# Performance work log

Hardware: AMD Instinct MI355X
Metric: run time of the kernel (lower is better)

The kernel has to match this reference:

```python
import jax, jax.numpy as jnp
import numpy as np


def setup_inputs() -> dict:
    key = jax.random.key(0)
    k1, k2 = jax.random.split(key)
    B, T, F = 8, 1000, 257
    m = jax.random.normal(k1, (B, 27, T, F), dtype=jnp.float32)
    x = jax.random.normal(k2, (B, F, T, 2), dtype=jnp.float32)
    v = jnp.array([[1.0, -0.5, -0.5], [0.0, np.sqrt(3) / 2, -np.sqrt(3) / 2]], dtype=jnp.float32)
    return {"m": m, "x": x, "v": v}


def reference(m, x, v):
    B, C, T, F = m.shape
    # m -> (B, 3, 9, T, F); contract the complex-basis dim (3) with v rows
    m5 = m.reshape(B, 3, C // 3, T, F)
    H_real = jnp.einsum('k,bkntf->bntf', v[0], m5)  # (B, 9, T, F)
    H_imag = jnp.einsum('k,bkntf->bntf', v[1], m5)
    M_real = H_real.reshape(B, 3, 3, T, F)
    M_imag = H_imag.reshape(B, 3, 3, T, F)

    # x: (B,F,T,2) -> (B,2,T,F), pad: time causal (top=2), freq symmetric (1,1)
    xp = jnp.transpose(x, (0, 3, 2, 1))
    xp = jnp.pad(xp, ((0, 0), (0, 0), (2, 0), (1, 1)))
    # 3x3 unfold as 9 shifted views: (B, 2, 3, 3, T, F)
    xu = jnp.stack(
        [xp[:, :, i:i + T, j:j + F] for i in range(3) for j in range(3)],
        axis=2,
    ).reshape(B, 2, 3, 3, T, F)

    xr, xi = xu[:, 0], xu[:, 1]
    x_enh_real = jnp.sum(M_real * xr - M_imag * xi, axis=(1, 2))  # (B, T, F)
    x_enh_imag = jnp.sum(M_real * xi + M_imag * xr, axis=(1, 2))
    x_enh = jnp.stack([x_enh_real, x_enh_imag], axis=3)  # (B, T, F, 2)
    return jnp.transpose(x_enh, (0, 2, 1, 3))  # (B, F, T, 2)
```

## Files before the change

### kernel.cpp

```cpp
#include <hip/hip_runtime.h>


constexpr int B = 8, C = 27, T = 1000, F = 257;
constexpr int TCH = 8;
constexpr int NT  = T / TCH;
constexpr int GRP = 320;
constexpr int BLK = 3 * GRP;
constexpr int HROW = 6;
constexpr int RP   = 7;
constexpr int PLANE = 260 * RP;
constexpr int SLABP = 257;
constexpr size_t CS = (size_t)T * F;

__global__ __launch_bounds__(BLK, 8)
void ccm_kernel(const float* __restrict__ m,
                const float* __restrict__ x,
                float* __restrict__ out) {
    __shared__ float  xs[2 * PLANE];
    __shared__ float2 rs[3 * TCH * SLABP];

    const int bid = blockIdx.x;
    const int tc  = bid % NT;
    const int b   = bid / NT;
    const int t0  = tc * TCH;
    const int tx  = threadIdx.x;
    const int g   = tx / GRP;
    const int f   = tx - g * GRP;
    const bool active = (f < F);

    const float* xb = x + (size_t)b * F * T * 2;

    const float SQ3_2 = 0.8660254037844386f;
    const float ckr = (g == 0) ? 1.0f : -0.5f;
    const float cki = (g == 0) ? 0.0f : ((g == 1) ? SQ3_2 : -SQ3_2);

    const float* mb = m + (((size_t)b * C + 9 * g) * T + t0) * F;

    float Am[9], Bm[9];
    float wr[3][3], wi[3][3];

    auto stage = [&](int tb) {
        for (int p = tx; p < 259 * HROW; p += BLK) {
            const int row = p / HROW;
            const int tt  = p - row * HROW;
            const int ff  = row - 1;
            const int t   = tb + tt;
            float re = 0.f, im = 0.f;
            if (ff >= 0 && ff < F && t >= 0) {
                const float2 v = *reinterpret_cast<const float2*>(
                    xb + ((size_t)ff * T + t) * 2);
                re = v.x; im = v.y;
            }
            xs[row * RP + tt]         = re;
            xs[PLANE + row * RP + tt] = im;
        }
    };

#define LOADM(DST, S)                                                     \
    {                                                                     \
        _Pragma("unroll")                                                 \
        for (int n = 0; n < 9; ++n)                                       \
            DST[n] = mb[(size_t)n * CS + (size_t)(S) * F + f];            \
    }

#define STEP(AV, S, U)                                                    \
    {                                                                     \
        _Pragma("unroll")                                                 \
        for (int j = 0; j < 3; ++j) {                                     \
            const float xr = xs[(f + j) * RP + ((U) + 2)];                \
            const float xi = xs[PLANE + (f + j) * RP + ((U) + 2)];        \
            wr[2][j] = ckr * xr - cki * xi;                               \
            wi[2][j] = ckr * xi + cki * xr;                               \
        }                                                                 \
        float accr = 0.f, acci = 0.f;                                     \
        _Pragma("unroll")                                                 \
        for (int i = 0; i < 3; ++i) {                                     \
            _Pragma("unroll")                                             \
            for (int j = 0; j < 3; ++j) {                                 \
                const int n = i * 3 + j;                                  \
                accr += AV[n] * wr[i][j];                                 \
                acci += AV[n] * wi[i][j];                                 \
            }                                                             \
        }                                                                 \
        rs[g * (TCH * SLABP) + (S) * SLABP + f] = make_float2(accr, acci);\
        _Pragma("unroll")                                                 \
        for (int j = 0; j < 3; ++j) {                                     \
            wr[0][j] = wr[1][j]; wi[0][j] = wi[1][j];                     \
            wr[1][j] = wr[2][j]; wi[1][j] = wi[2][j];                     \
        }                                                                 \
    }

    if (active) {
        LOADM(Am, 0);
        LOADM(Bm, 1);
    }
    stage(t0 - 2);
    __syncthreads();

    if (active) {
        #pragma unroll
        for (int p = 0; p < 2; ++p) {
            #pragma unroll
            for (int j = 0; j < 3; ++j) {
                const float xr = xs[(f + j) * RP + p];
                const float xi = xs[PLANE + (f + j) * RP + p];
                wr[p][j] = ckr * xr - cki * xi;
                wi[p][j] = ckr * xi + cki * xr;
            }
        }
        STEP(Am, 0, 0);  LOADM(Am, 2);
        STEP(Bm, 1, 1);  LOADM(Bm, 3);
        STEP(Am, 2, 2);  LOADM(Am, 4);
        STEP(Bm, 3, 3);  LOADM(Bm, 5);
    }
    __syncthreads();

    stage(t0 + 2);
    __syncthreads();

    if (active) {
        STEP(Am, 4, 0);  LOADM(Am, 6);
        STEP(Bm, 5, 1);  LOADM(Bm, 7);
        STEP(Am, 6, 2);
        STEP(Bm, 7, 3);
    }
#undef LOADM
#undef STEP
    __syncthreads();

    for (int task = tx; task < F * 4; task += BLK) {
        const int ff = task >> 2;
        const int q  = task & 3;
        float4 o = make_float4(0.f, 0.f, 0.f, 0.f);
        #pragma unroll
        for (int gg = 0; gg < 3; ++gg) {
            const float2 p0 = rs[gg * (TCH * SLABP) + (2 * q) * SLABP + ff];
            const float2 p1 = rs[gg * (TCH * SLABP) + (2 * q + 1) * SLABP + ff];
            o.x += p0.x; o.y += p0.y; o.z += p1.x; o.w += p1.y;
        }
        *reinterpret_cast<float4*>(
            out + ((size_t)(b * F + ff) * T + t0) * 2 + q * 4) = o;
    }
}

extern "C" void kernel_launch(void* const* d_in, const int* in_sizes, int n_in,
                              void* d_out, int out_size, void* d_ws, size_t ws_size,
                              hipStream_t stream) {
    const float* m = (const float*)d_in[0];
    const float* x = (const float*)d_in[1];
    float* out = (float*)d_out;

    const int grid = B * NT;
    ccm_kernel<<<grid, BLK, 0, stream>>>(m, x, out);
}
```

Baseline: 66.14 us.

## Halve time chunk per block and stage the x halo in a single pass

The time chunk per block drops from 8 to 4 steps, which doubles the grid and removes the second x-staging phase along with its extra barriers. The x halo (6 time rows) is loaded once at kernel start and overlaps with the m register prefetches. A third register buffer lets three m slices be in flight at once. In exchange, x halo reuse per block falls and there are twice as many blocks to launch.

```diff
diff --git a/kernel.cpp b/kernel.cpp
--- a/kernel.cpp
+++ b/kernel.cpp
@@ -2,12 +2,13 @@
 
 
 constexpr int B = 8, C = 27, T = 1000, F = 257;
-constexpr int TCH = 8;
+constexpr int TCH = 4;
 constexpr int NT  = T / TCH;
 constexpr int GRP = 320;
 constexpr int BLK = 3 * GRP;
-constexpr int HROW = 6;
-constexpr int RP   = 7;
+constexpr int TROW  = TCH + 2;
+constexpr int ROWSU = 259;
+constexpr int RP    = 7;
 constexpr int PLANE = 260 * RP;
 constexpr int SLABP = 257;
 constexpr size_t CS = (size_t)T * F;
@@ -30,31 +31,29 @@
 
     const float* xb = x + (size_t)b * F * T * 2;
 
+    for (int p = tx; p < ROWSU * TROW; p += BLK) {
+        const int row = p / TROW;
+        const int tt  = p - row * TROW;
+        const int ff  = row - 1;
+        const int t   = t0 - 2 + tt;
+        float re = 0.f, im = 0.f;
+        if (ff >= 0 && ff < F && t >= 0) {
+            const float2 v = *reinterpret_cast<const float2*>(
+                xb + ((size_t)ff * T + t) * 2);
+            re = v.x; im = v.y;
+        }
+        xs[row * RP + tt]         = re;
+        xs[PLANE + row * RP + tt] = im;
+    }
+
     const float SQ3_2 = 0.8660254037844386f;
     const float ckr = (g == 0) ? 1.0f : -0.5f;
     const float cki = (g == 0) ? 0.0f : ((g == 1) ? SQ3_2 : -SQ3_2);
 
     const float* mb = m + (((size_t)b * C + 9 * g) * T + t0) * F;
 
-    float Am[9], Bm[9];
+    float Am[9], Bm[9], Cm[9];
     float wr[3][3], wi[3][3];
-
-    auto stage = [&](int tb) {
-        for (int p = tx; p < 259 * HROW; p += BLK) {
-            const int row = p / HROW;
-            const int tt  = p - row * HROW;
-            const int ff  = row - 1;
-            const int t   = tb + tt;
-            float re = 0.f, im = 0.f;
-            if (ff >= 0 && ff < F && t >= 0) {
-                const float2 v = *reinterpret_cast<const float2*>(
-                    xb + ((size_t)ff * T + t) * 2);
-                re = v.x; im = v.y;
-            }
-            xs[row * RP + tt]         = re;
-            xs[PLANE + row * RP + tt] = im;
-        }
-    };
 
 #define LOADM(DST, S)                                                     \
     {                                                                     \
@@ -63,12 +62,12 @@
             DST[n] = mb[(size_t)n * CS + (size_t)(S) * F + f];            \
     }
 
-#define STEP(AV, S, U)                                                    \
+#define STEP(AV, S)                                                       \
     {                                                                     \
         _Pragma("unroll")                                                 \
         for (int j = 0; j < 3; ++j) {                                     \
-            const float xr = xs[(f + j) * RP + ((U) + 2)];                \
-            const float xi = xs[PLANE + (f + j) * RP + ((U) + 2)];        \
+            const float xr = xs[(f + j) * RP + ((S) + 2)];                \
+            const float xi = xs[PLANE + (f + j) * RP + ((S) + 2)];        \
             wr[2][j] = ckr * xr - cki * xi;                               \
             wi[2][j] = ckr * xi + cki * xr;                               \
         }                                                                 \
@@ -93,8 +92,8 @@
     if (active) {
         LOADM(Am, 0);
         LOADM(Bm, 1);
+        LOADM(Cm, 2);
     }
-    stage(t0 - 2);
     __syncthreads();
 
     if (active) {
@@ -108,29 +107,20 @@
                 wi[p][j] = ckr * xi + cki * xr;
             }
         }
-        STEP(Am, 0, 0);  LOADM(Am, 2);
-        STEP(Bm, 1, 1);  LOADM(Bm, 3);
-        STEP(Am, 2, 2);  LOADM(Am, 4);
-        STEP(Bm, 3, 3);  LOADM(Bm, 5);
-    }
-    __syncthreads();
 
-    stage(t0 + 2);
-    __syncthreads();
-
-    if (active) {
-        STEP(Am, 4, 0);  LOADM(Am, 6);
-        STEP(Bm, 5, 1);  LOADM(Bm, 7);
-        STEP(Am, 6, 2);
-        STEP(Bm, 7, 3);
+        STEP(Am, 0);  LOADM(Am, 3);
+        STEP(Bm, 1);
+        STEP(Cm, 2);
+        STEP(Am, 3);
     }
 #undef LOADM
 #undef STEP
+
     __syncthreads();
 
-    for (int task = tx; task < F * 4; task += BLK) {
-        const int ff = task >> 2;
-        const int q  = task & 3;
+    if (tx < F * 2) {
+        const int ff = tx >> 1;
+        const int q  = tx & 1;
         float4 o = make_float4(0.f, 0.f, 0.f, 0.f);
         #pragma unroll
         for (int gg = 0; gg < 3; ++gg) {
```

After: 124.9 us. +88.9%, slower.
